# Performance work log

Hardware: AMD Instinct MI355X
Metric: run time of the kernel (lower is better)

The kernel has to match this reference:

```python
import jax, jax.numpy as jnp
import numpy as np

B, S, D, H = 2, 2048, 1024, 16
DK = D // H
SCALE = 1.0 / np.sqrt(DK).astype(np.float32)


def setup_inputs() -> dict:
    key = jax.random.key(0)
    ks = jax.random.split(key, 7)
    std = 1.0 / np.sqrt(D).astype(np.float32)
    return {
        "query": jax.random.normal(ks[0], (B, S, D), jnp.float32),
        "key": jax.random.normal(ks[1], (B, S, D), jnp.float32),
        "value": jax.random.normal(ks[2], (B, S, D), jnp.float32),
        "Wq": jax.random.normal(ks[3], (D, D), jnp.float32) * std,
        "Wk": jax.random.normal(ks[4], (D, D), jnp.float32) * std,
        "Wv": jax.random.normal(ks[5], (D, D), jnp.float32) * std,
        "Wo": jax.random.normal(ks[6], (D, D), jnp.float32) * std,
    }


def _split_heads(x):
    # [B, S, D] -> [B, H, S, DK]
    return x.reshape(B, S, H, DK).transpose(0, 2, 1, 3)


def reference(query, key, value, Wq, Wk, Wv, Wo):
    Q = _split_heads(query @ Wq)
    K = _split_heads(key @ Wk)
    V = _split_heads(value @ Wv)
    # explicit full-score attention, as in the original (mask=None, dropout off)
    scores = jnp.einsum("bhqd,bhkd->bhqk", Q, K) * SCALE
    attn = jax.nn.softmax(scores, axis=-1)
    out = jnp.einsum("bhqk,bhkd->bhqd", attn, V)
    out = out.transpose(0, 2, 1, 3).reshape(B, S, D)  # merge heads
    return out @ Wo
```

## Files before the change

kernel.cpp:

```cpp
#include <hip/hip_runtime.h>

#define B_ 2
#define S_ 2048
#define D_ 1024
#define H_ 16

typedef unsigned short u16;
typedef unsigned long long u64;
typedef __bf16 bf16x8 __attribute__((ext_vector_type(8)));
typedef float f32x4 __attribute__((ext_vector_type(4)));
typedef unsigned short u16x8 __attribute__((ext_vector_type(8)));
typedef unsigned short u16x4 __attribute__((ext_vector_type(4)));
typedef unsigned uint4v __attribute__((ext_vector_type(4)));

__device__ __forceinline__ unsigned swz128(unsigned o) {
  return o ^ (((o >> 7) & 7) << 4);
}
__device__ __forceinline__ unsigned swz256(unsigned o) {
  return o ^ (((o >> 8) & 7) << 4);
}

__device__ __forceinline__ unsigned xcd_swz(unsigned id, unsigned cpx) {
  return (id & 7) * cpx + (id >> 3);
}

__device__ __forceinline__ void gload_lds16(const void* g, void* l) {
  __builtin_amdgcn_global_load_lds(
      (const __attribute__((address_space(1))) unsigned*)g,
      (__attribute__((address_space(3))) unsigned*)l, 16, 0, 0);
}

__device__ __forceinline__ u16 f2bf(float f) {
  union { float f; unsigned u; } v;
  v.f = f;
  unsigned u = v.u;
  return (u16)((u + 0x7fffu + ((u >> 16) & 1u)) >> 16);
}

__device__ __forceinline__ unsigned cvtpk(float lo, float hi) {
  unsigned d;
  asm("v_cvt_pk_bf16_f32 %0, %1, %2" : "=v"(d) : "v"(lo), "v"(hi));
  return d;
}

__device__ __forceinline__ float max3f(float a, float b, float c) {
  float d;
  asm("v_max3_f32 %0, %1, %2, %3" : "=v"(d) : "v"(a), "v"(b), "v"(c));
  return d;
}

struct T4 { const float* in[4]; u16* out[4]; };
__global__ __launch_bounds__(256) void transpose_w4(T4 p) {
  __shared__ u16 t[64][65];
  const float* in = p.in[blockIdx.z];
  u16* out = p.out[blockIdx.z];
  int r0 = blockIdx.y * 64, c0 = blockIdx.x * 64;
  for (int i = threadIdx.x; i < 4096; i += 256) {
    int r = i >> 6, c = i & 63;
    t[r][c] = f2bf(in[(size_t)(r0 + r) * 1024 + c0 + c]);
  }
  __syncthreads();
  for (int i = threadIdx.x; i < 4096; i += 256) {
    int r = i >> 6, c = i & 63;
    out[(size_t)(c0 + r) * 1024 + r0 + c] = t[c][r];
  }
}

struct QKV { const float* A[3]; const u16* BT[3]; u16* C[2]; u16* VT; };
__global__ __launch_bounds__(256) void gemm_qkv(QKV p) {
  constexpr int K = 1024, N = 1024;
  __shared__ __align__(16) u16 lbuf[2][128 * 64];
  const int tid = threadIdx.x, lane = tid & 63, w = tid >> 6;
  const int wr = w >> 1, wc = w & 1;
  const int z = blockIdx.z;
  const int m0 = blockIdx.x * 128, n0 = blockIdx.y * 128;
  const int g = lane >> 4, c16 = lane & 15;
  f32x4 acc[4][4] = {};
  const float* Af = p.A[z] + (size_t)m0 * K;
  const char* Bb = (const char*)(p.BT[z] + (size_t)n0 * K);
  char* lAb = (char*)lbuf[0];
  char* lBb = (char*)lbuf[1];
  for (int kt = 0; kt < K; kt += 64) {
    for (int c = 0; c < 4; ++c) {
      unsigned o = c * 4096 + tid * 16;
      unsigned u = swz128(o);
      gload_lds16(Bb + (size_t)(u >> 7) * (K * 2) + kt * 2 + (u & 127), lBb + o);
    }
    for (int c = 0; c < 4; ++c) {
      unsigned o = c * 4096 + tid * 16;
      unsigned row = o >> 7, kc = (o & 127) >> 1;
      const float* s = Af + (size_t)row * K + kt + kc;
      float4 f0 = *(const float4*)s;
      float4 f1 = *(const float4*)(s + 4);
      uint4v d;
      d[0] = cvtpk(f0.x, f0.y);
      d[1] = cvtpk(f0.z, f0.w);
      d[2] = cvtpk(f1.x, f1.y);
      d[3] = cvtpk(f1.z, f1.w);
      *(uint4v*)(lAb + swz128(o)) = d;
    }
    asm volatile("s_waitcnt vmcnt(0)" ::: "memory");
    __syncthreads();
    for (int ks = 0; ks < 2; ++ks) {
      bf16x8 af[4], bf[4];
      for (int i = 0; i < 4; ++i) {
        unsigned row = wr * 64 + i * 16 + c16;
        unsigned o = row * 128 + ks * 64 + g * 16;
        af[i] = *(const bf16x8*)(lAb + (o ^ ((row & 7) << 4)));
      }
      for (int j = 0; j < 4; ++j) {
        unsigned row = wc * 64 + j * 16 + c16;
        unsigned o = row * 128 + ks * 64 + g * 16;
        bf[j] = *(const bf16x8*)(lBb + (o ^ ((row & 7) << 4)));
      }
      for (int i = 0; i < 4; ++i)
        for (int j = 0; j < 4; ++j)
          acc[i][j] = __builtin_amdgcn_mfma_f32_16x16x32_bf16(af[i], bf[j],
                                                              acc[i][j], 0, 0, 0);
    }
    __syncthreads();
  }
  if (z < 2) {
    u16* C = p.C[z];
    for (int i = 0; i < 4; ++i)
      for (int j = 0; j < 4; ++j) {
        int row = m0 + wr * 64 + i * 16 + g * 4;
        int col = n0 + wc * 64 + j * 16 + c16;
        for (int r = 0; r < 4; ++r)
          C[(size_t)(row + r) * N + col] = f2bf(acc[i][j][r]);
      }
  } else {
    char* Tb = (char*)lbuf;
    for (int i = 0; i < 4; ++i)
      for (int j = 0; j < 4; ++j) {
        unsigned s_local = wr * 64 + i * 16 + g * 4;
        unsigned dk_col = wc * 64 + j * 16 + c16;
        unsigned o = dk_col * 256 + s_local * 2;
        u16x4 ov;
        ov[0] = f2bf(acc[i][j][0]);
        ov[1] = f2bf(acc[i][j][1]);
        ov[2] = f2bf(acc[i][j][2]);
        ov[3] = f2bf(acc[i][j][3]);
        *(u16x4*)(Tb + swz256(o)) = ov;
      }
    __syncthreads();
    const int b = m0 >> 11, s0blk = m0 & 2047;
    for (int c = 0; c < 8; ++c) {
      unsigned idx = c * 4096 + tid * 16;
      unsigned row = idx >> 8, off = idx & 255;
      int h = (n0 + (int)row) >> 6, dk = (n0 + (int)row) & 63;
      int bh = b * 16 + h;
      char* dst = (char*)p.VT + (((size_t)bh * 64 + dk) * S_ + s0blk) * 2 + off;
      *(u16x8*)dst = *(const u16x8*)(Tb + swz256(idx));
    }
  }
}

__global__ __launch_bounds__(256) void gemm_bt_f32(const u16* __restrict__ A,
                                                   const u16* __restrict__ BT,
                                                   float* __restrict__ C) {
  constexpr int K = 1024, N = 1024;
  __shared__ __align__(16) u16 lA[128 * 64];
  __shared__ __align__(16) u16 lB[128 * 64];
  const int tid = threadIdx.x, lane = tid & 63, w = tid >> 6;
  const int wr = w >> 1, wc = w & 1;
  const int m0 = blockIdx.x * 128, n0 = blockIdx.y * 128;
  const int g = lane >> 4, c16 = lane & 15;
  f32x4 acc[4][4] = {};
  const char* Ab = (const char*)(A + (size_t)m0 * K);
  const char* Bb = (const char*)(BT + (size_t)n0 * K);
  char* lAb = (char*)lA;
  char* lBb = (char*)lB;
  for (int kt = 0; kt < K; kt += 64) {
    for (int c = 0; c < 4; ++c) {
      unsigned o = c * 4096 + tid * 16;
      unsigned u = swz128(o);
      gload_lds16(Ab + (size_t)(u >> 7) * (K * 2) + kt * 2 + (u & 127), lAb + o);
      gload_lds16(Bb + (size_t)(u >> 7) * (K * 2) + kt * 2 + (u & 127), lBb + o);
    }
    asm volatile("s_waitcnt vmcnt(0)" ::: "memory");
    __syncthreads();
    for (int ks = 0; ks < 2; ++ks) {
      bf16x8 af[4], bf[4];
      for (int i = 0; i < 4; ++i) {
        unsigned row = wr * 64 + i * 16 + c16;
        unsigned o = row * 128 + ks * 64 + g * 16;
        af[i] = *(const bf16x8*)(lAb + (o ^ ((row & 7) << 4)));
      }
      for (int j = 0; j < 4; ++j) {
        unsigned row = wc * 64 + j * 16 + c16;
        unsigned o = row * 128 + ks * 64 + g * 16;
        bf[j] = *(const bf16x8*)(lBb + (o ^ ((row & 7) << 4)));
      }
      for (int i = 0; i < 4; ++i)
        for (int j = 0; j < 4; ++j)
          acc[i][j] = __builtin_amdgcn_mfma_f32_16x16x32_bf16(af[i], bf[j],
                                                              acc[i][j], 0, 0, 0);
    }
    __syncthreads();
  }
  for (int i = 0; i < 4; ++i)
    for (int j = 0; j < 4; ++j) {
      int row = m0 + wr * 64 + i * 16 + g * 4;
      int col = n0 + wc * 64 + j * 16 + c16;
      for (int r = 0; r < 4; ++r)
        C[(size_t)(row + r) * N + col] = acc[i][j][r];
    }
}

__global__ __launch_bounds__(256) void flash_attn(const u16* __restrict__ Q,
                                                  const u16* __restrict__ K,
                                                  const u16* __restrict__ VT,
                                                  u16* __restrict__ O) {
  __shared__ __align__(16) u16 lP[64 * 64];
  __shared__ __align__(16) u16 lK[2][64 * 64];
  __shared__ __align__(16) u16 lV[2][64 * 64];
  const int tid = threadIdx.x, lane = tid & 63, w = tid >> 6;
  const int g = lane >> 4, c16 = lane & 15;
  unsigned id = blockIdx.x + blockIdx.y * gridDim.x;
  unsigned sw = xcd_swz(id, 128);
  const int q0 = (sw & 31) * 64;
  const int bh = sw >> 5, b = bh >> 4, h = bh & 15;
  const char* Qb = (const char*)(Q + (size_t)(b * S_ + q0) * D_ + h * 64);
  const char* Kb = (const char*)(K + (size_t)b * S_ * D_ + h * 64);
  const char* Vb = (const char*)(VT + (size_t)bh * 64 * S_);
  char* lPb = (char*)lP;
  char* lKb = (char*)lK;
  char* lVb = (char*)lV;

  const unsigned mask = (c16 & 7) << 4;
  const unsigned fb0 = c16 * 128 + ((g * 16) ^ mask);
  const unsigned fb1 = c16 * 128 + ((64 + g * 16) ^ mask);
  unsigned uo[2];
  for (int c = 0; c < 2; ++c) uo[c] = swz128(w * 2048 + c * 1024 + lane * 16);

  for (int c = 0; c < 2; ++c) {
    unsigned u = uo[c];
    char* dst = (char*)(w * 2048 + c * 1024);
    gload_lds16(Qb + (size_t)(u >> 7) * (D_ * 2) + (u & 127), lPb + (size_t)dst);
    gload_lds16(Kb + (size_t)(u >> 7) * (D_ * 2) + (u & 127), lKb + (size_t)dst);
    gload_lds16(Vb + (size_t)(u >> 7) * (S_ * 2) + (u & 127), lVb + (size_t)dst);
  }
  float m_run = -INFINITY, l_run = 0.f;
  f32x4 oacc[4] = {};
  asm volatile("s_waitcnt vmcnt(0)" ::: "memory");
  __syncthreads();
  bf16x8 qf[2];
  qf[0] = *(const bf16x8*)(lPb + w * 2048 + fb0);
  qf[1] = *(const bf16x8*)(lPb + w * 2048 + fb1);
  const float SC2 = 0.125f * 1.44269504088896340736f;
  const unsigned qrow = w * 16 + c16;
  const unsigned pw = qrow * 128 + ((g * 8) ^ (mask & 16));
  const unsigned mh = mask & 96;
  int cur = 0;
  for (int kv0 = 0; kv0 < S_; kv0 += 64, cur ^= 1) {
    const char* curK = lKb + cur * 8192;
    const char* curV = lVb + cur * 8192;
    if (kv0 + 64 < S_) {
      char* nK = lKb + (cur ^ 1) * 8192;
      char* nV = lVb + (cur ^ 1) * 8192;
      for (int c = 0; c < 2; ++c) {
        unsigned u = uo[c];
        unsigned dst = w * 2048 + c * 1024;
        gload_lds16(Kb + (size_t)(kv0 + 64 + (u >> 7)) * (D_ * 2) + (u & 127),
                    nK + dst);
        gload_lds16(Vb + (size_t)(u >> 7) * (S_ * 2) + (size_t)(kv0 + 64) * 2 + (u & 127),
                    nV + dst);
      }
    }
    f32x4 s[4] = {};
    __builtin_amdgcn_s_setprio(1);
    for (int j = 0; j < 4; ++j) {
      bf16x8 kf = *(const bf16x8*)(curK + fb0 + j * 2048);
      s[j] = __builtin_amdgcn_mfma_f32_16x16x32_bf16(kf, qf[0], s[j], 0, 0, 0);
    }
    for (int j = 0; j < 4; ++j) {
      bf16x8 kf = *(const bf16x8*)(curK + fb1 + j * 2048);
      s[j] = __builtin_amdgcn_mfma_f32_16x16x32_bf16(kf, qf[1], s[j], 0, 0, 0);
    }
    __builtin_amdgcn_s_setprio(0);
    float t0 = max3f(s[0][0], s[0][1], s[0][2]);
    float t1 = max3f(s[0][3], s[1][0], s[1][1]);
    float t2 = max3f(s[1][2], s[1][3], s[2][0]);
    float t3 = max3f(s[2][1], s[2][2], s[2][3]);
    float t4 = max3f(s[3][0], s[3][1], s[3][2]);
    float rm = fmaxf(max3f(t0, t1, t2), max3f(t3, t4, s[3][3]));
    rm = fmaxf(rm, __shfl_xor(rm, 16));
    rm = fmaxf(rm, __shfl_xor(rm, 32));
    if (!__all((rm - m_run) * SC2 <= 8.0f)) {
      float mn = fmaxf(m_run, rm);
      float sc = exp2f((m_run - mn) * SC2);
      l_run *= sc;
      for (int i = 0; i < 4; ++i) oacc[i] *= sc;
      m_run = mn;
    }
    float rsj[4];
    for (int j = 0; j < 4; ++j) {
      float p0 = exp2f((s[j][0] - m_run) * SC2);
      float p1 = exp2f((s[j][1] - m_run) * SC2);
      float p2 = exp2f((s[j][2] - m_run) * SC2);
      float p3 = exp2f((s[j][3] - m_run) * SC2);
      rsj[j] = (p0 + p1) + (p2 + p3);
      unsigned w0 = cvtpk(p0, p1);
      unsigned w1 = cvtpk(p2, p3);
      *(u64*)(lPb + pw + ((unsigned)(j * 32) ^ mh)) = (u64)w0 | ((u64)w1 << 32);
    }
    float rs = (rsj[0] + rsj[1]) + (rsj[2] + rsj[3]);
    rs += __shfl_xor(rs, 16);
    rs += __shfl_xor(rs, 32);
    l_run += rs;
    __builtin_amdgcn_s_setprio(1);
    {
      bf16x8 pf0 = *(const bf16x8*)(lPb + w * 2048 + fb0);
      for (int i = 0; i < 4; ++i) {
        bf16x8 vf = *(const bf16x8*)(curV + fb0 + i * 2048);
        oacc[i] = __builtin_amdgcn_mfma_f32_16x16x32_bf16(vf, pf0, oacc[i], 0, 0, 0);
      }
      bf16x8 pf1 = *(const bf16x8*)(lPb + w * 2048 + fb1);
      for (int i = 0; i < 4; ++i) {
        bf16x8 vf = *(const bf16x8*)(curV + fb1 + i * 2048);
        oacc[i] = __builtin_amdgcn_mfma_f32_16x16x32_bf16(vf, pf1, oacc[i], 0, 0, 0);
      }
    }
    __builtin_amdgcn_s_setprio(0);
    asm volatile("s_waitcnt vmcnt(0)" ::: "memory");
    __syncthreads();
  }
  float inv = 1.f / l_run;
  int q = q0 + w * 16 + c16;
  u16* orow = O + (size_t)(b * S_ + q) * D_ + h * 64;
  for (int i = 0; i < 4; ++i) {
    unsigned e0 = cvtpk(oacc[i][0] * inv, oacc[i][1] * inv);
    unsigned e1 = cvtpk(oacc[i][2] * inv, oacc[i][3] * inv);
    *(u64*)(orow + i * 16 + g * 4) = (u64)e0 | ((u64)e1 << 32);
  }
}

extern "C" void kernel_launch(void* const* d_in, const int* in_sizes, int n_in,
                              void* d_out, int out_size, void* d_ws, size_t ws_size,
                              hipStream_t stream) {
  const float* q_in = (const float*)d_in[0];
  const float* k_in = (const float*)d_in[1];
  const float* v_in = (const float*)d_in[2];
  const float* Wq = (const float*)d_in[3];
  const float* Wk = (const float*)d_in[4];
  const float* Wv = (const float*)d_in[5];
  const float* Wo = (const float*)d_in[6];
  u16* ws = (u16*)d_ws;
  const size_t WSZ = (size_t)1024 * 1024;
  const size_t TSZ = (size_t)B_ * S_ * D_;
  u16* WqT = ws;
  u16* WkT = ws + WSZ;
  u16* WvT = ws + 2 * WSZ;
  u16* WoT = ws + 3 * WSZ;
  u16* Qb = ws + 4 * WSZ;
  u16* Kb = Qb + TSZ;
  u16* VTb = Kb + TSZ;
  u16* Ob = VTb + TSZ;
  dim3 tb(256);
  T4 tw = {{Wq, Wk, Wv, Wo}, {WqT, WkT, WvT, WoT}};
  transpose_w4<<<dim3(16, 16, 4), tb, 0, stream>>>(tw);
  QKV gq = {{q_in, k_in, v_in}, {WqT, WkT, WvT}, {Qb, Kb}, VTb};
  gemm_qkv<<<dim3(32, 8, 3), tb, 0, stream>>>(gq);
  flash_attn<<<dim3(32, 32), tb, 0, stream>>>(Qb, Kb, VTb, Ob);
  gemm_bt_f32<<<dim3(32, 8), tb, 0, stream>>>(Ob, WoT, (float*)d_out);
}
```

Measured before the change: 160.2 us.

## Load V fragments directly from global in attention and halve output GEMM N-tile

```diff
diff --git a/kernel.cpp b/kernel.cpp
--- a/kernel.cpp
+++ b/kernel.cpp
@@ -161,48 +161,54 @@
                                                    float* __restrict__ C) {
   constexpr int K = 1024, N = 1024;
   __shared__ __align__(16) u16 lA[128 * 64];
-  __shared__ __align__(16) u16 lB[128 * 64];
+  __shared__ __align__(16) u16 lB[64 * 64];
   const int tid = threadIdx.x, lane = tid & 63, w = tid >> 6;
   const int wr = w >> 1, wc = w & 1;
-  const int m0 = blockIdx.x * 128, n0 = blockIdx.y * 128;
+  const int m0 = blockIdx.x * 128, n0 = blockIdx.y * 64;
   const int g = lane >> 4, c16 = lane & 15;
-  f32x4 acc[4][4] = {};
+  f32x4 acc[4][2] = {};
   const char* Ab = (const char*)(A + (size_t)m0 * K);
   const char* Bb = (const char*)(BT + (size_t)n0 * K);
   char* lAb = (char*)lA;
   char* lBb = (char*)lB;
   for (int kt = 0; kt < K; kt += 64) {
     for (int c = 0; c < 4; ++c) {
-      unsigned o = c * 4096 + tid * 16;
+      unsigned o = w * 4096 + c * 1024 + lane * 16;
       unsigned u = swz128(o);
-      gload_lds16(Ab + (size_t)(u >> 7) * (K * 2) + kt * 2 + (u & 127), lAb + o);
-      gload_lds16(Bb + (size_t)(u >> 7) * (K * 2) + kt * 2 + (u & 127), lBb + o);
+      gload_lds16(Ab + (size_t)(u >> 7) * (K * 2) + kt * 2 + (u & 127),
+                  lAb + w * 4096 + c * 1024);
+    }
+    for (int c = 0; c < 2; ++c) {
+      unsigned o = w * 2048 + c * 1024 + lane * 16;
+      unsigned u = swz128(o);
+      gload_lds16(Bb + (size_t)(u >> 7) * (K * 2) + kt * 2 + (u & 127),
+                  lBb + w * 2048 + c * 1024);
     }
     asm volatile("s_waitcnt vmcnt(0)" ::: "memory");
     __syncthreads();
     for (int ks = 0; ks < 2; ++ks) {
-      bf16x8 af[4], bf[4];
+      bf16x8 af[4], bf[2];
       for (int i = 0; i < 4; ++i) {
         unsigned row = wr * 64 + i * 16 + c16;
         unsigned o = row * 128 + ks * 64 + g * 16;
         af[i] = *(const bf16x8*)(lAb + (o ^ ((row & 7) << 4)));
       }
-      for (int j = 0; j < 4; ++j) {
-        unsigned row = wc * 64 + j * 16 + c16;
+      for (int j = 0; j < 2; ++j) {
+        unsigned row = wc * 32 + j * 16 + c16;
         unsigned o = row * 128 + ks * 64 + g * 16;
         bf[j] = *(const bf16x8*)(lBb + (o ^ ((row & 7) << 4)));
       }
       for (int i = 0; i < 4; ++i)
-        for (int j = 0; j < 4; ++j)
+        for (int j = 0; j < 2; ++j)
           acc[i][j] = __builtin_amdgcn_mfma_f32_16x16x32_bf16(af[i], bf[j],
                                                               acc[i][j], 0, 0, 0);
     }
     __syncthreads();
   }
   for (int i = 0; i < 4; ++i)
-    for (int j = 0; j < 4; ++j) {
+    for (int j = 0; j < 2; ++j) {
       int row = m0 + wr * 64 + i * 16 + g * 4;
-      int col = n0 + wc * 64 + j * 16 + c16;
+      int col = n0 + wc * 32 + j * 16 + c16;
       for (int r = 0; r < 4; ++r)
         C[(size_t)(row + r) * N + col] = acc[i][j][r];
     }
@@ -214,7 +220,6 @@
                                                   u16* __restrict__ O) {
   __shared__ __align__(16) u16 lP[64 * 64];
   __shared__ __align__(16) u16 lK[2][64 * 64];
-  __shared__ __align__(16) u16 lV[2][64 * 64];
   const int tid = threadIdx.x, lane = tid & 63, w = tid >> 6;
   const int g = lane >> 4, c16 = lane & 15;
   unsigned id = blockIdx.x + blockIdx.y * gridDim.x;
@@ -226,7 +231,6 @@
   const char* Vb = (const char*)(VT + (size_t)bh * 64 * S_);
   char* lPb = (char*)lP;
   char* lKb = (char*)lK;
-  char* lVb = (char*)lV;
 
   const unsigned mask = (c16 & 7) << 4;
   const unsigned fb0 = c16 * 128 + ((g * 16) ^ mask);
@@ -236,10 +240,9 @@
 
   for (int c = 0; c < 2; ++c) {
     unsigned u = uo[c];
-    char* dst = (char*)(w * 2048 + c * 1024);
-    gload_lds16(Qb + (size_t)(u >> 7) * (D_ * 2) + (u & 127), lPb + (size_t)dst);
-    gload_lds16(Kb + (size_t)(u >> 7) * (D_ * 2) + (u & 127), lKb + (size_t)dst);
-    gload_lds16(Vb + (size_t)(u >> 7) * (S_ * 2) + (u & 127), lVb + (size_t)dst);
+    unsigned dst = w * 2048 + c * 1024;
+    gload_lds16(Qb + (size_t)(u >> 7) * (D_ * 2) + (u & 127), lPb + dst);
+    gload_lds16(Kb + (size_t)(u >> 7) * (D_ * 2) + (u & 127), lKb + dst);
   }
   float m_run = -INFINITY, l_run = 0.f;
   f32x4 oacc[4] = {};
@@ -252,22 +255,22 @@
   const unsigned qrow = w * 16 + c16;
   const unsigned pw = qrow * 128 + ((g * 8) ^ (mask & 16));
   const unsigned mh = mask & 96;
+  const char* Vrow = Vb + ((size_t)c16 * S_ + g * 8) * 2;
   int cur = 0;
   for (int kv0 = 0; kv0 < S_; kv0 += 64, cur ^= 1) {
     const char* curK = lKb + cur * 8192;
-    const char* curV = lVb + cur * 8192;
     if (kv0 + 64 < S_) {
       char* nK = lKb + (cur ^ 1) * 8192;
-      char* nV = lVb + (cur ^ 1) * 8192;
       for (int c = 0; c < 2; ++c) {
         unsigned u = uo[c];
-        unsigned dst = w * 2048 + c * 1024;
         gload_lds16(Kb + (size_t)(kv0 + 64 + (u >> 7)) * (D_ * 2) + (u & 127),
-                    nK + dst);
-        gload_lds16(Vb + (size_t)(u >> 7) * (S_ * 2) + (size_t)(kv0 + 64) * 2 + (u & 127),
-                    nV + dst);
-      }
-    }
+                    nK + w * 2048 + c * 1024);
+      }
+    }
+    bf16x8 vf[8];
+    for (int ks = 0; ks < 2; ++ks)
+      for (int i = 0; i < 4; ++i)
+        vf[ks * 4 + i] = *(const bf16x8*)(Vrow + ((size_t)i * 16 * S_ + kv0 + ks * 32) * 2);
     f32x4 s[4] = {};
     __builtin_amdgcn_s_setprio(1);
     for (int j = 0; j < 4; ++j) {
@@ -305,27 +308,22 @@
       unsigned w1 = cvtpk(p2, p3);
       *(u64*)(lPb + pw + ((unsigned)(j * 32) ^ mh)) = (u64)w0 | ((u64)w1 << 32);
     }
-    float rs = (rsj[0] + rsj[1]) + (rsj[2] + rsj[3]);
-    rs += __shfl_xor(rs, 16);
-    rs += __shfl_xor(rs, 32);
-    l_run += rs;
+    l_run += (rsj[0] + rsj[1]) + (rsj[2] + rsj[3]);
     __builtin_amdgcn_s_setprio(1);
     {
       bf16x8 pf0 = *(const bf16x8*)(lPb + w * 2048 + fb0);
-      for (int i = 0; i < 4; ++i) {
-        bf16x8 vf = *(const bf16x8*)(curV + fb0 + i * 2048);
-        oacc[i] = __builtin_amdgcn_mfma_f32_16x16x32_bf16(vf, pf0, oacc[i], 0, 0, 0);
-      }
+      for (int i = 0; i < 4; ++i)
+        oacc[i] = __builtin_amdgcn_mfma_f32_16x16x32_bf16(vf[i], pf0, oacc[i], 0, 0, 0);
       bf16x8 pf1 = *(const bf16x8*)(lPb + w * 2048 + fb1);
-      for (int i = 0; i < 4; ++i) {
-        bf16x8 vf = *(const bf16x8*)(curV + fb1 + i * 2048);
-        oacc[i] = __builtin_amdgcn_mfma_f32_16x16x32_bf16(vf, pf1, oacc[i], 0, 0, 0);
-      }
+      for (int i = 0; i < 4; ++i)
+        oacc[i] = __builtin_amdgcn_mfma_f32_16x16x32_bf16(vf[4 + i], pf1, oacc[i], 0, 0, 0);
     }
     __builtin_amdgcn_s_setprio(0);
     asm volatile("s_waitcnt vmcnt(0)" ::: "memory");
     __syncthreads();
   }
+  l_run += __shfl_xor(l_run, 16);
+  l_run += __shfl_xor(l_run, 32);
   float inv = 1.f / l_run;
   int q = q0 + w * 16 + c16;
   u16* orow = O + (size_t)(b * S_ + q) * D_ + h * 64;
@@ -363,5 +361,5 @@
   QKV gq = {{q_in, k_in, v_in}, {WqT, WkT, WvT}, {Qb, Kb}, VTb};
   gemm_qkv<<<dim3(32, 8, 3), tb, 0, stream>>>(gq);
   flash_attn<<<dim3(32, 32), tb, 0, stream>>>(Qb, Kb, VTb, Ob);
-  gemm_bt_f32<<<dim3(32, 8), tb, 0, stream>>>(Ob, WoT, (float*)d_out);
-}
+  gemm_bt_f32<<<dim3(32, 16), tb, 0, stream>>>(Ob, WoT, (float*)d_out);
+}
```

After: 211.2 us. 31.8% more time.
